# Optimization experiments

Hardware: AMD Instinct MI355X
Metric: run time of the kernel (lower is better)

The kernel has to match this reference:

```python
import jax, jax.numpy as jnp
import numpy as np

EPS = 1e-5  # BatchNorm eps
K_NN = 16


def _conv1d(w, b, x):
    # 1x1 Conv1d: w (O,C), x (B,C,N) -> (B,O,N)
    return jnp.einsum('oc,bcn->bon', w, x) + b[None, :, None]


def _conv2d(w, b, x):
    # 1x1 Conv2d: w (O,C), x (B,C,N,K) -> (B,O,N,K)
    return jnp.einsum('oc,bcnk->bonk', w, x) + b[None, :, None, None]


def _bn2d(x, g, bt, mu, var):
    # eval-mode BatchNorm2d over channel axis 1
    inv = g / jnp.sqrt(var + EPS)
    return x * inv[None, :, None, None] + (bt - mu * inv)[None, :, None, None]


def _group(f, idx):
    # grouping_operation: f (B,C,M), idx (B,N,K) -> (B,C,N,K)
    return jax.vmap(lambda fb, ib: fb[:, ib])(f, idx)


def _knn(query_pts, ref_pts, k):
    # query (B,N,3), ref (B,M,3) -> k nearest ref indices per query (B,N,k)
    d = (jnp.sum(query_pts ** 2, -1)[:, :, None]
         + jnp.sum(ref_pts ** 2, -1)[:, None, :]
         - 2.0 * jnp.einsum('bnc,bmc->bnm', query_pts, ref_pts))
    _, idx = jax.lax.top_k(-d, k)
    return idx


def setup_inputs() -> dict:
    key = jax.random.key(0)
    B, n, m, C, D, PH = 4, 4096, 1024, 128, 256, 64
    AH = 2 * D
    ks = iter(jax.random.split(key, 40))

    def nrm(shape, scale):
        return jax.random.normal(next(ks), shape, jnp.float32) * scale

    pos = nrm((B, 3, n), 1.0)
    return {
        'pos': pos,
        'pos_flipped': jnp.transpose(pos, (0, 2, 1)),
        'fea': nrm((B, C, n), 1.0),
        'seed': nrm((B, m, 3), 1.0),
        'seed_fea': nrm((B, C, m), 1.0),
        'w_start': nrm((D, C), C ** -0.5), 'b_start': jnp.zeros((D,), jnp.float32),
        'w_key': nrm((D, D), D ** -0.5), 'b_key': jnp.zeros((D,), jnp.float32),
        'w_value': nrm((D, D), D ** -0.5), 'b_value': jnp.zeros((D,), jnp.float32),
        'w_query': nrm((D, C), C ** -0.5), 'b_query': jnp.zeros((D,), jnp.float32),
        'pos_w1': nrm((PH, 4), 0.5), 'pos_b1': jnp.zeros((PH,), jnp.float32),
        'pos_g1': jnp.ones((PH,), jnp.float32), 'pos_beta1': jnp.zeros((PH,), jnp.float32),
        'pos_mu1': jnp.zeros((PH,), jnp.float32), 'pos_var1': jnp.ones((PH,), jnp.float32),
        'pos_w2': nrm((D, PH), PH ** -0.5), 'pos_b2': jnp.zeros((D,), jnp.float32),
        'attn_w1': nrm((AH, D), D ** -0.5), 'attn_b1': jnp.zeros((AH,), jnp.float32),
        'attn_g1': jnp.ones((AH,), jnp.float32), 'attn_beta1': jnp.zeros((AH,), jnp.float32),
        'attn_mu1': jnp.zeros((AH,), jnp.float32), 'attn_var1': jnp.ones((AH,), jnp.float32),
        'attn_w2': nrm((D, AH), AH ** -0.5), 'attn_b2': jnp.zeros((D,), jnp.float32),
        'w_end': nrm((C, D), D ** -0.5), 'b_end': jnp.zeros((C,), jnp.float32),
    }


def reference(pos, pos_flipped, fea, seed, seed_fea,
              w_start, b_start, w_key, b_key, w_value, b_value, w_query, b_query,
              pos_w1, pos_b1, pos_g1, pos_beta1, pos_mu1, pos_var1, pos_w2, pos_b2,
              attn_w1, attn_b1, attn_g1, attn_beta1, attn_mu1, attn_var1, attn_w2, attn_b2,
              w_end, b_end):
    value = _conv1d(w_start, b_start, seed_fea)                    # (B,D,m)
    idx = _knn(jax.lax.stop_gradient(pos_flipped),
               jax.lax.stop_gradient(seed), K_NN)                  # (B,n,K) no-grad topk
    key_f = _conv1d(w_key, b_key, value)
    val_f = _conv1d(w_value, b_value, value)
    query = _conv1d(w_query, b_query, fea)                         # (B,D,n)
    key_g = _group(key_f, idx)                                     # (B,D,n,K)
    qk_rel = query[:, :, :, None] - key_g
    val_g = _group(val_f, idx)                                     # (B,D,n,K)
    coord_xj = _group(jnp.transpose(seed, (0, 2, 1)), idx)         # (B,3,n,K)
    pos_rel = pos[:, :, :, None] - coord_xj                        # (B,3,n,K)
    dis = jnp.linalg.norm(pos_rel, axis=1, keepdims=True)          # (B,1,n,K)
    h = jnp.concatenate([dis, pos_rel], axis=1)                    # (B,4,n,K)
    pe = _conv2d(pos_w2, pos_b2,
                 jax.nn.relu(_bn2d(_conv2d(pos_w1, pos_b1, h),
                                   pos_g1, pos_beta1, pos_mu1, pos_var1)))  # (B,D,n,K)
    hid = jax.nn.relu(_bn2d(_conv2d(attn_w1, attn_b1, qk_rel + pe),
                            attn_g1, attn_beta1, attn_mu1, attn_var1))
    weights = jax.nn.softmax(_conv2d(attn_w2, attn_b2, hid), axis=-1)  # softmax over K
    agg = jnp.einsum('bcnk,bcnk->bcn', weights, val_g + pe)        # (B,D,n)
    return _conv1d(w_end, b_end, agg) + fea                        # (B,C,n)
```

## Files before the change

kernel.cpp:

```cpp
#include <hip/hip_runtime.h>
#include <hip/hip_bf16.h>

#define BB   4
#define NQ   4096
#define MS   1024
#define CF   128
#define DD   256
#define PHH  64
#define AHH  512
#define KNN  16
#define EPSBN 1e-5f
#define LDH  72
#define LKH  264

typedef unsigned short ushort_t;
typedef __attribute__((ext_vector_type(8))) short bf16x8;
typedef __attribute__((ext_vector_type(4))) float floatx4;

__device__ __forceinline__ float u2f(ushort_t u) {
  return __uint_as_float(((unsigned int)u) << 16);
}
__device__ __forceinline__ ushort_t f2u(float f) {
  __hip_bfloat16 h = __float2bfloat16(f);
  return *(ushort_t*)&h;
}

#define NSEG 30
struct CvtArgs {
  const void* src[NSEG];
  int cnt[NSEG];
  int off[NSEG];
};

__global__ __launch_bounds__(256) void cvt_kernel(CvtArgs a, float* __restrict__ dst,
                                                  const ushort_t* __restrict__ probe) {
  const bool f32 = (probe[0] == 0);
  const int gid = blockIdx.x * 256 + threadIdx.x;
  const int gsz = gridDim.x * 256;
  for (int s = 0; s < NSEG; ++s) {
    float* d = dst + a.off[s];
    const int n = a.cnt[s];
    if (f32) {
      const float* sp = (const float*)a.src[s];
      for (int i = gid; i < n; i += gsz) d[i] = sp[i];
    } else {
      const ushort_t* sp = (const ushort_t*)a.src[s];
      for (int i = gid; i < n; i += gsz) d[i] = u2f(sp[i]);
    }
  }
}

__global__ __launch_bounds__(256) void cvtw_kernel(
    const float* __restrict__ w1f, const float* __restrict__ w2f,
    const float* __restrict__ w2pf,
    ushort_t* __restrict__ w1b, ushort_t* __restrict__ w2b,
    ushort_t* __restrict__ w2pb) {
  int i = blockIdx.x * 256 + threadIdx.x;
  w1b[i] = f2u(w1f[i]);
  w2b[i] = f2u(w2f[i]);
  if (i < DD * PHH) w2pb[i] = f2u(w2pf[i]);
}

__global__ __launch_bounds__(128) void prep_kernel(
    const float* __restrict__ w1f, const float* __restrict__ w2pf,
    const float* __restrict__ wqf, const float* __restrict__ bqf,
    const float* __restrict__ b2f, const float* __restrict__ ab1f,
    ushort_t* __restrict__ WWb, ushort_t* __restrict__ WQHb,
    float* __restrict__ ballf) {
  __shared__ float s_w1[DD];
  const int a = blockIdx.x;
  const int t = threadIdx.x;
  s_w1[t] = w1f[a * DD + t];
  s_w1[t + 128] = w1f[a * DD + t + 128];
  __syncthreads();
  {
    float acc = 0.f;
    for (int d = 0; d < DD; ++d) acc += s_w1[d] * wqf[d * CF + t];
    WQHb[a * CF + t] = f2u(acc);
  }
  if (t < PHH) {
    float acc = 0.f;
    for (int d = 0; d < DD; ++d) acc += s_w1[d] * w2pf[d * PHH + t];
    WWb[a * PHH + t] = f2u(acc);
  }
  if (t == 0) {
    float acc = ab1f[a];
    for (int d = 0; d < DD; ++d) acc += s_w1[d] * (bqf[d] + b2f[d]);
    ballf[a] = acc;
  }
}

__global__ __launch_bounds__(256) void vkv_kernel(
    const float* __restrict__ w_start, const float* __restrict__ b_start,
    const float* __restrict__ w_key, const float* __restrict__ b_key,
    const float* __restrict__ w_value, const float* __restrict__ b_value,
    const float* __restrict__ seed_fea,
    ushort_t* __restrict__ key_b, ushort_t* __restrict__ val_b) {
  __shared__ __align__(16) float s_val[4][DD];
  const int tid = threadIdx.x;
  const int b = blockIdx.x >> 8;
  const int m0 = (blockIdx.x & 255) << 2;

  float a0 = b_start[tid], a1 = a0, a2 = a0, a3 = a0;
  {
    const float* wrow = w_start + tid * CF;
    const float* colb = seed_fea + b * CF * MS + m0;
    for (int c = 0; c < CF; c += 4) {
      float4 w = *(const float4*)(wrow + c);
      float4 f0 = *(const float4*)(colb + (c + 0) * MS);
      float4 f1 = *(const float4*)(colb + (c + 1) * MS);
      float4 f2 = *(const float4*)(colb + (c + 2) * MS);
      float4 f3 = *(const float4*)(colb + (c + 3) * MS);
      a0 += w.x * f0.x + w.y * f1.x + w.z * f2.x + w.w * f3.x;
      a1 += w.x * f0.y + w.y * f1.y + w.z * f2.y + w.w * f3.y;
      a2 += w.x * f0.z + w.y * f1.z + w.z * f2.z + w.w * f3.z;
      a3 += w.x * f0.w + w.y * f1.w + w.z * f2.w + w.w * f3.w;
    }
  }
  s_val[0][tid] = a0; s_val[1][tid] = a1; s_val[2][tid] = a2; s_val[3][tid] = a3;
  __syncthreads();

  float ak[4], av[4];
#pragma unroll
  for (int i = 0; i < 4; ++i) { ak[i] = b_key[tid]; av[i] = b_value[tid]; }
  {
    const float* kr = w_key + tid * DD;
    const float* vr = w_value + tid * DD;
    for (int c = 0; c < DD; c += 4) {
      float4 ku = *(const float4*)(kr + c);
      float4 vu = *(const float4*)(vr + c);
      float4 v0 = *(const float4*)(&s_val[0][c]);
      float4 v1 = *(const float4*)(&s_val[1][c]);
      float4 v2 = *(const float4*)(&s_val[2][c]);
      float4 v3 = *(const float4*)(&s_val[3][c]);
      ak[0] += ku.x * v0.x + ku.y * v0.y + ku.z * v0.z + ku.w * v0.w;
      ak[1] += ku.x * v1.x + ku.y * v1.y + ku.z * v1.z + ku.w * v1.w;
      ak[2] += ku.x * v2.x + ku.y * v2.y + ku.z * v2.z + ku.w * v2.w;
      ak[3] += ku.x * v3.x + ku.y * v3.y + ku.z * v3.z + ku.w * v3.w;
      av[0] += vu.x * v0.x + vu.y * v0.y + vu.z * v0.z + vu.w * v0.w;
      av[1] += vu.x * v1.x + vu.y * v1.y + vu.z * v1.z + vu.w * v1.w;
      av[2] += vu.x * v2.x + vu.y * v2.y + vu.z * v2.z + vu.w * v2.w;
      av[3] += vu.x * v3.x + vu.y * v3.y + vu.z * v3.z + vu.w * v3.w;
    }
  }
#pragma unroll
  for (int i = 0; i < 4; ++i) {
    key_b[(b * MS + m0 + i) * DD + tid] = f2u(ak[i]);
    val_b[(b * MS + m0 + i) * DD + tid] = f2u(av[i]);
  }
}

__global__ __launch_bounds__(256) void kh_kernel(
    const ushort_t* __restrict__ key_b, const ushort_t* __restrict__ w1b,
    ushort_t* __restrict__ khb) {
  __shared__ __align__(16) ushort_t s_key[16 * LKH];
  const int tid = threadIdx.x;
  const int wv = tid >> 6, ln = tid & 63;
  const int qu = ln >> 4, l15 = ln & 15;
  const int b = blockIdx.x >> 6;
  const int m0 = (blockIdx.x & 63) << 4;
  {
    const int row = tid >> 4, seg = tid & 15;
    const ushort_t* src = key_b + (b * MS + m0 + row) * DD + seg * 16;
    ushort_t* dst = s_key + row * LKH + seg * 16;
    *(bf16x8*)(dst + 0) = *(const bf16x8*)(src + 0);
    *(bf16x8*)(dst + 8) = *(const bf16x8*)(src + 8);
  }
  __syncthreads();
  bf16x8 af[8];
#pragma unroll
  for (int ks = 0; ks < 8; ++ks)
    af[ks] = *(const bf16x8*)(s_key + l15 * LKH + ks * 32 + qu * 8);
  floatx4 acc[8];
#pragma unroll
  for (int nt = 0; nt < 8; ++nt) acc[nt] = (floatx4){0.f, 0.f, 0.f, 0.f};
#pragma unroll
  for (int ks = 0; ks < 8; ++ks)
#pragma unroll
    for (int nt = 0; nt < 8; ++nt) {
      bf16x8 bfr = *(const bf16x8*)(w1b + (wv * 128 + nt * 16 + l15) * DD + ks * 32 + qu * 8);
      acc[nt] = __builtin_amdgcn_mfma_f32_16x16x32_bf16(af[ks], bfr, acc[nt], 0, 0, 0);
    }
#pragma unroll
  for (int nt = 0; nt < 8; ++nt)
#pragma unroll
    for (int r = 0; r < 4; ++r)
      khb[(b * MS + m0 + qu * 4 + r) * AHH + wv * 128 + nt * 16 + l15] = f2u(acc[nt][r]);
}

__global__ __launch_bounds__(512) void knn_kernel(
    const float* __restrict__ pos_flipped, const float* __restrict__ seed,
    int* __restrict__ idx_out) {
  __shared__ float s_p[MS * 3];
  const int tid = threadIdx.x;
  const int wv = tid >> 6, ln = tid & 63;
  const int b = blockIdx.x >> 9;
  const int q = ((blockIdx.x & 511) << 3) + wv;

  for (int i = tid; i < MS * 3; i += 512) s_p[i] = seed[b * MS * 3 + i];
  __syncthreads();

  const float qx = pos_flipped[(b * NQ + q) * 3 + 0];
  const float qy = pos_flipped[(b * NQ + q) * 3 + 1];
  const float qz = pos_flipped[(b * NQ + q) * 3 + 2];
  const float q2 = qx * qx + qy * qy + qz * qz;

  unsigned long long key[16];
#pragma unroll
  for (int t = 0; t < 16; ++t) {
    int j = ln + (t << 6);
    float x = s_p[j * 3 + 0], y = s_p[j * 3 + 1], z = s_p[j * 3 + 2];
    float r2 = x * x + y * y + z * z;
    float dist = q2 + r2 - 2.0f * (qx * x + qy * y + qz * z);
    unsigned u = __float_as_uint(dist);
    u ^= (u >> 31) ? 0xFFFFFFFFu : 0x80000000u;
    key[t] = ((unsigned long long)u << 10) | (unsigned)j;
  }

#pragma unroll 1
  for (int r = 0; r < KNN; ++r) {
    unsigned long long m = key[0];
#pragma unroll
    for (int t = 1; t < 16; ++t) m = (key[t] < m) ? key[t] : m;
#pragma unroll
    for (int off = 32; off >= 1; off >>= 1) {
      unsigned lo = (unsigned)m, hi = (unsigned)(m >> 32);
      unsigned olo = __shfl_xor((int)lo, off);
      unsigned ohi = __shfl_xor((int)hi, off);
      unsigned long long o = ((unsigned long long)ohi << 32) | olo;
      m = (o < m) ? o : m;
    }
    if (ln == 0) idx_out[(b * NQ + q) * KNN + r] = (int)(m & 1023u);
#pragma unroll
    for (int t = 0; t < 16; ++t) key[t] = (key[t] == m) ? ~0ull : key[t];
  }
}

__global__ __launch_bounds__(256, 4) void fused_kernel(
    const float* __restrict__ pos, const float* __restrict__ seed,
    const void* __restrict__ fea_raw,
    const float* __restrict__ pos_w1, const float* __restrict__ pos_b1,
    const float* __restrict__ pos_g1, const float* __restrict__ pos_beta1,
    const float* __restrict__ pos_mu1, const float* __restrict__ pos_var1,
    const ushort_t* __restrict__ w2pb, const float* __restrict__ pos_b2,
    const float* __restrict__ attn_g1, const float* __restrict__ attn_beta1,
    const float* __restrict__ attn_mu1, const float* __restrict__ attn_var1,
    const float* __restrict__ ballf,
    const ushort_t* __restrict__ WWb, const ushort_t* __restrict__ WQHb,
    const ushort_t* __restrict__ w2b, const ushort_t* __restrict__ khb,
    const ushort_t* __restrict__ val_b,
    const int* __restrict__ idx_in,
    const float* __restrict__ w_end, const float* __restrict__ b_end,
    void* __restrict__ out_raw, const ushort_t* __restrict__ probe) {
  __shared__ __align__(16) ushort_t s_phb[64 * LDH];
  __shared__ __align__(16) ushort_t s_hid[64 * LDH];
  __shared__ __align__(16) float s_qh[4 * AHH];
  __shared__ __align__(16) ushort_t s_feab[4 * CF];
  __shared__ float s_h[64 * 4];
  __shared__ int s_idx[64];

  float* s_agg = s_qh;

  const int tid = threadIdx.x;
  const int wv = tid >> 6;
  const int ln = tid & 63;
  const int qu = ln >> 4, l15 = ln & 15;
  const bool f32io = (probe[0] == 0);
  const int q0 = blockIdx.x * 4;
  const int b = q0 >> 12;
  const int qn0 = q0 & (NQ - 1);

  if (tid < 64) {
    const int g = tid >> 4;
    const int qn = qn0 + g;
    const int j = idx_in[(q0 + g) * KNN + (tid & 15)];
    s_idx[tid] = j;
    float px = pos[(b * 3 + 0) * NQ + qn];
    float py = pos[(b * 3 + 1) * NQ + qn];
    float pz = pos[(b * 3 + 2) * NQ + qn];
    float rx = px - seed[(b * MS + j) * 3 + 0];
    float ry = py - seed[(b * MS + j) * 3 + 1];
    float rz = pz - seed[(b * MS + j) * 3 + 2];
    float dis = sqrtf(rx * rx + ry * ry + rz * rz);
    s_h[tid * 4 + 0] = dis;
    s_h[tid * 4 + 1] = rx;
    s_h[tid * 4 + 2] = ry;
    s_h[tid * 4 + 3] = rz;
  }
  if (tid < 128) {
    const int c = tid;
    if (f32io) {
      const float* fc = (const float*)fea_raw + (size_t)b * CF * NQ + (size_t)c * NQ + qn0;
      float4 v = *(const float4*)fc;
      s_feab[0 * CF + c] = f2u(v.x);
      s_feab[1 * CF + c] = f2u(v.y);
      s_feab[2 * CF + c] = f2u(v.z);
      s_feab[3 * CF + c] = f2u(v.w);
    } else {
      const ushort_t* fc = (const ushort_t*)fea_raw + (size_t)b * CF * NQ + (size_t)c * NQ + qn0;
      unsigned long long v = *(const unsigned long long*)fc;
      s_feab[0 * CF + c] = (ushort_t)(v);
      s_feab[1 * CF + c] = (ushort_t)(v >> 16);
      s_feab[2 * CF + c] = (ushort_t)(v >> 32);
      s_feab[3 * CF + c] = (ushort_t)(v >> 48);
    }
  }
  __syncthreads();

  {
    const int p = tid & 63, kb = tid >> 6;
    float4 w = *(const float4*)(pos_w1 + p * 4);
    float inv = pos_g1[p] * rsqrtf(pos_var1[p] + EPSBN);
    float off = pos_b1[p] * inv + pos_beta1[p] - pos_mu1[p] * inv;
#pragma unroll
    for (int i = 0; i < 16; ++i) {
      int gk = kb * 16 + i;
      float raw = w.x * s_h[gk * 4 + 0] + w.y * s_h[gk * 4 + 1] +
                  w.z * s_h[gk * 4 + 2] + w.w * s_h[gk * 4 + 3];
      s_phb[gk * LDH + p] = f2u(fmaxf(raw * inv + off, 0.0f));
    }
  }

  {
    bf16x8 afq[4];
#pragma unroll
    for (int ks = 0; ks < 4; ++ks) {
      if (l15 < 4) afq[ks] = *(const bf16x8*)(s_feab + l15 * CF + ks * 32 + qu * 8);
      else afq[ks] = (bf16x8){0, 0, 0, 0, 0, 0, 0, 0};
    }
    floatx4 aq[8];
#pragma unroll
    for (int nt = 0; nt < 8; ++nt) aq[nt] = (floatx4){0.f, 0.f, 0.f, 0.f};
#pragma unroll
    for (int ks = 0; ks < 4; ++ks)
#pragma unroll
      for (int nt = 0; nt < 8; ++nt) {
        bf16x8 bfr = *(const bf16x8*)(WQHb + (nt * 64 + wv * 16 + l15) * CF + ks * 32 + qu * 8);
        aq[nt] = __builtin_amdgcn_mfma_f32_16x16x32_bf16(afq[ks], bfr, aq[nt], 0, 0, 0);
      }
    if (qu == 0) {
#pragma unroll
      for (int nt = 0; nt < 8; ++nt)
#pragma unroll
        for (int r = 0; r < 4; ++r)
          s_qh[r * AHH + nt * 64 + wv * 16 + l15] = aq[nt][r];
    }
  }
  __syncthreads();

  floatx4 accl[4][4];
#pragma unroll
  for (int mt = 0; mt < 4; ++mt)
#pragma unroll
    for (int nt = 0; nt < 4; ++nt) accl[mt][nt] = (floatx4){0.f, 0.f, 0.f, 0.f};

#pragma unroll 1
  for (int nc = 0; nc < 8; ++nc) {
    {
      floatx4 accb[4];
#pragma unroll
      for (int mt = 0; mt < 4; ++mt) accb[mt] = (floatx4){0.f, 0.f, 0.f, 0.f};
#pragma unroll
      for (int ks = 0; ks < 2; ++ks) {
        bf16x8 bw = *(const bf16x8*)(WWb + (nc * 64 + wv * 16 + l15) * PHH + ks * 32 + qu * 8);
#pragma unroll
        for (int mt = 0; mt < 4; ++mt) {
          bf16x8 af = *(const bf16x8*)(s_phb + (mt * 16 + l15) * LDH + ks * 32 + qu * 8);
          accb[mt] = __builtin_amdgcn_mfma_f32_16x16x32_bf16(af, bw, accb[mt], 0, 0, 0);
        }
      }
      const int a = nc * 64 + wv * 16 + l15;
      float inv = attn_g1[a] * rsqrtf(attn_var1[a] + EPSBN);
      float offc = ballf[a] * inv + attn_beta1[a] - attn_mu1[a] * inv;
#pragma unroll
      for (int mt = 0; mt < 4; ++mt) {
        const float qhv = s_qh[mt * AHH + a];
#pragma unroll
        for (int r = 0; r < 4; ++r) {
          const int row = mt * 16 + qu * 4 + r;
          float khv = u2f(khb[(b * MS + s_idx[row]) * AHH + a]);
          float raw = accb[mt][r] + qhv - khv;
          s_hid[row * LDH + wv * 16 + l15] = f2u(fmaxf(raw * inv + offc, 0.0f));
        }
      }
    }
    __syncthreads();
    {
#pragma unroll
      for (int ks = 0; ks < 2; ++ks) {
        bf16x8 af2[4];
#pragma unroll
        for (int mt = 0; mt < 4; ++mt)
          af2[mt] = *(const bf16x8*)(s_hid + (mt * 16 + l15) * LDH + ks * 32 + qu * 8);
#pragma unroll
        for (int nt = 0; nt < 4; ++nt) {
          bf16x8 bfr = *(const bf16x8*)(w2b + (wv * 64 + nt * 16 + l15) * AHH +
                                        nc * 64 + ks * 32 + qu * 8);
#pragma unroll
          for (int mt = 0; mt < 4; ++mt)
            accl[mt][nt] = __builtin_amdgcn_mfma_f32_16x16x32_bf16(af2[mt], bfr, accl[mt][nt], 0, 0, 0);
        }
      }
    }
    __syncthreads();
  }

#pragma unroll
  for (int nt = 0; nt < 4; ++nt) {
    const int c = wv * 64 + nt * 16 + l15;
    floatx4 ap[4];
#pragma unroll
    for (int mt = 0; mt < 4; ++mt) ap[mt] = (floatx4){0.f, 0.f, 0.f, 0.f};
#pragma unroll
    for (int ks = 0; ks < 2; ++ks) {
      bf16x8 bfr = *(const bf16x8*)(w2pb + c * PHH + ks * 32 + qu * 8);
#pragma unroll
      for (int mt = 0; mt < 4; ++mt) {
        bf16x8 af = *(const bf16x8*)(s_phb + (mt * 16 + l15) * LDH + ks * 32 + qu * 8);
        ap[mt] = __builtin_amdgcn_mfma_f32_16x16x32_bf16(af, bfr, ap[mt], 0, 0, 0);
      }
    }
    const float b2v = pos_b2[c];
#pragma unroll
    for (int mt = 0; mt < 4; ++mt) {
      float l0 = accl[mt][nt][0], l1 = accl[mt][nt][1];
      float l2 = accl[mt][nt][2], l3 = accl[mt][nt][3];
      float mx = fmaxf(fmaxf(l0, l1), fmaxf(l2, l3));
      mx = fmaxf(mx, __shfl_xor(mx, 16));
      mx = fmaxf(mx, __shfl_xor(mx, 32));
      float e0 = expf(l0 - mx), e1 = expf(l1 - mx);
      float e2 = expf(l2 - mx), e3 = expf(l3 - mx);
      float s = e0 + e1 + e2 + e3;
      s += __shfl_xor(s, 16);
      s += __shfl_xor(s, 32);
      const int row0 = mt * 16 + qu * 4;
      float v0 = u2f(val_b[(b * MS + s_idx[row0 + 0]) * DD + c]);
      float v1 = u2f(val_b[(b * MS + s_idx[row0 + 1]) * DD + c]);
      float v2 = u2f(val_b[(b * MS + s_idx[row0 + 2]) * DD + c]);
      float v3 = u2f(val_b[(b * MS + s_idx[row0 + 3]) * DD + c]);
      float p = e0 * (v0 + ap[mt][0] + b2v) + e1 * (v1 + ap[mt][1] + b2v) +
                e2 * (v2 + ap[mt][2] + b2v) + e3 * (v3 + ap[mt][3] + b2v);
      p += __shfl_xor(p, 16);
      p += __shfl_xor(p, 32);
      if (ln < 16) s_agg[mt * DD + c] = p / s;
    }
  }
  __syncthreads();

  {
    const int c = tid & 127;
    const int qh = tid >> 7;
    float acc0 = 0.0f, acc1 = 0.0f;
    const float* wr = w_end + c * DD;
    for (int d = 0; d < DD; d += 4) {
      float4 w4 = *(const float4*)(wr + d);
      float4 a0 = *(const float4*)(s_agg + (qh + 0) * DD + d);
      float4 a1 = *(const float4*)(s_agg + (qh + 2) * DD + d);
      acc0 += w4.x * a0.x + w4.y * a0.y + w4.z * a0.z + w4.w * a0.w;
      acc1 += w4.x * a1.x + w4.y * a1.y + w4.z * a1.z + w4.w * a1.w;
    }
    const float be = b_end[c];
#pragma unroll
    for (int t = 0; t < 2; ++t) {
      const int q = qh + t * 2;
      const float accv = (t == 0) ? acc0 : acc1;
      const int oidx = (b * CF + c) * NQ + qn0 + q;
      float fres = f32io ? ((const float*)fea_raw)[oidx]
                         : u2f(((const ushort_t*)fea_raw)[oidx]);
      float v = accv + be + fres;
      if (f32io) ((float*)out_raw)[oidx] = v;
      else ((ushort_t*)out_raw)[oidx] = f2u(v);
    }
  }
}

extern "C" void kernel_launch(void* const* d_in, const int* in_sizes, int n_in,
                              void* d_out, int out_size, void* d_ws, size_t ws_size,
                              hipStream_t stream) {
  (void)in_sizes; (void)n_in; (void)out_size; (void)ws_size;

  float* wsf = (float*)d_ws;
  ushort_t* key_b = (ushort_t*)wsf;
  ushort_t* val_b = (ushort_t*)(wsf + 524288);
  int*      idxw  = (int*)(wsf + 1048576);
  float*    nrm   = wsf + 1310720;
  ushort_t* w1b   = (ushort_t*)(wsf + 2458304);
  ushort_t* w2b   = (ushort_t*)(wsf + 2523840);
  ushort_t* w2pb  = (ushort_t*)(wsf + 2589376);
  ushort_t* khb   = (ushort_t*)(wsf + 2613952);
  ushort_t* WWb   = (ushort_t*)(wsf + 3662528);
  ushort_t* WQHb  = (ushort_t*)(wsf + 3678912);
  float*    ballf = wsf + 3711680;

  static const int seg_in[NSEG] = {0, 1, 3, 4, 5, 6, 7, 8, 9, 10, 11, 12, 13, 14,
                                   15, 16, 17, 18, 19, 20, 21, 22, 23, 24, 25, 26,
                                   27, 28, 29, 30};
  static const int seg_cnt[NSEG] = {
      49152, 49152, 12288, 524288, 32768, 256, 65536, 256, 65536, 256,
      32768, 256, 256, 64, 64, 64, 64, 64, 16384, 256,
      131072, 512, 512, 512, 512, 512, 131072, 256, 32768, 128};
  static const int seg_off[NSEG] = {
      0, 49152, 98304, 110592, 634880, 667648, 667904, 733440, 733696, 799232,
      799488, 832256, 832512, 832768, 832832, 832896, 832960, 833024, 833088, 849472,
      849728, 980800, 981312, 981824, 982336, 982848, 983360, 1114432, 1114688, 1147456};

  CvtArgs ca;
  for (int s = 0; s < NSEG; ++s) {
    ca.src[s] = d_in[seg_in[s]];
    ca.cnt[s] = seg_cnt[s];
    ca.off[s] = seg_off[s];
  }
  const ushort_t* probe = (const ushort_t*)d_in[18];

  const float* posN      = nrm + 0;
  const float* pos_flipN = nrm + 49152;
  const float* seedN     = nrm + 98304;
  const float* seed_feaN = nrm + 110592;
  const float* w_startN  = nrm + 634880;
  const float* b_startN  = nrm + 667648;
  const float* w_keyN    = nrm + 667904;
  const float* b_keyN    = nrm + 733440;
  const float* w_valueN  = nrm + 733696;
  const float* b_valueN  = nrm + 799232;
  const float* w_queryN  = nrm + 799488;
  const float* b_queryN  = nrm + 832256;
  const float* pos_w1N   = nrm + 832512;
  const float* pos_b1N   = nrm + 832768;
  const float* pos_g1N   = nrm + 832832;
  const float* pos_beta1N= nrm + 832896;
  const float* pos_mu1N  = nrm + 832960;
  const float* pos_var1N = nrm + 833024;
  const float* pos_w2N   = nrm + 833088;
  const float* pos_b2N   = nrm + 849472;
  const float* attn_w1N  = nrm + 849728;
  const float* attn_b1N  = nrm + 980800;
  const float* attn_g1N  = nrm + 981312;
  const float* attn_beta1N = nrm + 981824;
  const float* attn_mu1N = nrm + 982336;
  const float* attn_var1N= nrm + 982848;
  const float* attn_w2N  = nrm + 983360;
  const float* w_endN    = nrm + 1114688;
  const float* b_endN    = nrm + 1147456;

  cvt_kernel<<<512, 256, 0, stream>>>(ca, nrm, probe);
  cvtw_kernel<<<512, 256, 0, stream>>>(attn_w1N, attn_w2N, pos_w2N,
                                       w1b, w2b, w2pb);
  prep_kernel<<<512, 128, 0, stream>>>(attn_w1N, pos_w2N, w_queryN,
                                       b_queryN, pos_b2N, attn_b1N,
                                       WWb, WQHb, ballf);
  vkv_kernel<<<BB * MS / 4, 256, 0, stream>>>(w_startN, b_startN, w_keyN, b_keyN,
                                              w_valueN, b_valueN, seed_feaN,
                                              key_b, val_b);
  kh_kernel<<<BB * MS / 16, 256, 0, stream>>>(key_b, w1b, khb);
  knn_kernel<<<BB * NQ / 8, 512, 0, stream>>>(pos_flipN, seedN, idxw);

  fused_kernel<<<BB * NQ / 4, 256, 0, stream>>>(
      posN, seedN, d_in[2],
      pos_w1N, pos_b1N, pos_g1N, pos_beta1N, pos_mu1N, pos_var1N,
      w2pb, pos_b2N,
      attn_g1N, attn_beta1N, attn_mu1N, attn_var1N,
      ballf, WWb, WQHb, w2b, khb, val_b, idxw,
      w_endN, b_endN, d_out, probe);
}
```

Baseline: 747.6 us.

## Prefetch gathered key-hidden values one chunk ahead and raise occupancy bound

The gathered khb loads for the next hidden-channel chunk are now issued before the second GEMM of the current chunk. The values are packed two bf16 per register, and the loop is manually unrolled by two with ping-pong buffers. This is meant to hide the latency of the scattered global gather behind MFMA work. Launch bounds also move from 4 to 5 blocks per CU. That caps registers tighter and risks spills, especially with the extra prefetch registers and the 64-entry accl accumulators.

```diff
diff --git a/kernel.cpp b/kernel.cpp
--- a/kernel.cpp
+++ b/kernel.cpp
@@ -236,7 +236,7 @@
   }
 }
 
-__global__ __launch_bounds__(256, 4) void fused_kernel(
+__global__ __launch_bounds__(256, 5) void fused_kernel(
     const float* __restrict__ pos, const float* __restrict__ seed,
     const void* __restrict__ fea_raw,
     const float* __restrict__ pos_w1, const float* __restrict__ pos_b1,
@@ -354,54 +354,84 @@
 #pragma unroll
     for (int nt = 0; nt < 4; ++nt) accl[mt][nt] = (floatx4){0.f, 0.f, 0.f, 0.f};
 
+  auto ldkh = [&](int nc, unsigned (&pk)[8]) {
+    const int a = nc * 64 + wv * 16 + l15;
+#pragma unroll
+    for (int mt = 0; mt < 4; ++mt)
+#pragma unroll
+      for (int rp = 0; rp < 2; ++rp) {
+        const int row = mt * 16 + qu * 4 + rp * 2;
+        unsigned lo = khb[(b * MS + s_idx[row]) * AHH + a];
+        unsigned hi = khb[(b * MS + s_idx[row + 1]) * AHH + a];
+        pk[mt * 2 + rp] = lo | (hi << 16);
+      }
+  };
+
+  auto do_B = [&](int nc, const unsigned (&pk)[8]) {
+    floatx4 accb[4];
+#pragma unroll
+    for (int mt = 0; mt < 4; ++mt) accb[mt] = (floatx4){0.f, 0.f, 0.f, 0.f};
+#pragma unroll
+    for (int ks = 0; ks < 2; ++ks) {
+      bf16x8 bw = *(const bf16x8*)(WWb + (nc * 64 + wv * 16 + l15) * PHH + ks * 32 + qu * 8);
+#pragma unroll
+      for (int mt = 0; mt < 4; ++mt) {
+        bf16x8 af = *(const bf16x8*)(s_phb + (mt * 16 + l15) * LDH + ks * 32 + qu * 8);
+        accb[mt] = __builtin_amdgcn_mfma_f32_16x16x32_bf16(af, bw, accb[mt], 0, 0, 0);
+      }
+    }
+    const int a = nc * 64 + wv * 16 + l15;
+    float inv = attn_g1[a] * rsqrtf(attn_var1[a] + EPSBN);
+    float offc = ballf[a] * inv + attn_beta1[a] - attn_mu1[a] * inv;
+#pragma unroll
+    for (int mt = 0; mt < 4; ++mt) {
+      const float qhv = s_qh[mt * AHH + a];
+#pragma unroll
+      for (int rp = 0; rp < 2; ++rp) {
+        const float kh0 = u2f((ushort_t)(pk[mt * 2 + rp] & 0xFFFFu));
+        const float kh1 = u2f((ushort_t)(pk[mt * 2 + rp] >> 16));
+        const int row0 = mt * 16 + qu * 4 + rp * 2;
+        float raw0 = accb[mt][rp * 2 + 0] + qhv - kh0;
+        float raw1 = accb[mt][rp * 2 + 1] + qhv - kh1;
+        s_hid[(row0 + 0) * LDH + wv * 16 + l15] = f2u(fmaxf(raw0 * inv + offc, 0.0f));
+        s_hid[(row0 + 1) * LDH + wv * 16 + l15] = f2u(fmaxf(raw1 * inv + offc, 0.0f));
+      }
+    }
+  };
+
+  auto do_C = [&](int nc) {
+#pragma unroll
+    for (int ks = 0; ks < 2; ++ks) {
+      bf16x8 af2[4];
+#pragma unroll
+      for (int mt = 0; mt < 4; ++mt)
+        af2[mt] = *(const bf16x8*)(s_hid + (mt * 16 + l15) * LDH + ks * 32 + qu * 8);
+#pragma unroll
+      for (int nt = 0; nt < 4; ++nt) {
+        bf16x8 bfr = *(const bf16x8*)(w2b + (wv * 64 + nt * 16 + l15) * AHH +
+                                      nc * 64 + ks * 32 + qu * 8);
+#pragma unroll
+        for (int mt = 0; mt < 4; ++mt)
+          accl[mt][nt] = __builtin_amdgcn_mfma_f32_16x16x32_bf16(af2[mt], bfr, accl[mt][nt], 0, 0, 0);
+      }
+    }
+  };
+
+  unsigned pkA[8], pkB[8];
+  ldkh(0, pkA);
+
 #pragma unroll 1
-  for (int nc = 0; nc < 8; ++nc) {
-    {
-      floatx4 accb[4];
-#pragma unroll
-      for (int mt = 0; mt < 4; ++mt) accb[mt] = (floatx4){0.f, 0.f, 0.f, 0.f};
-#pragma unroll
-      for (int ks = 0; ks < 2; ++ks) {
-        bf16x8 bw = *(const bf16x8*)(WWb + (nc * 64 + wv * 16 + l15) * PHH + ks * 32 + qu * 8);
-#pragma unroll
-        for (int mt = 0; mt < 4; ++mt) {
-          bf16x8 af = *(const bf16x8*)(s_phb + (mt * 16 + l15) * LDH + ks * 32 + qu * 8);
-          accb[mt] = __builtin_amdgcn_mfma_f32_16x16x32_bf16(af, bw, accb[mt], 0, 0, 0);
-        }
-      }
-      const int a = nc * 64 + wv * 16 + l15;
-      float inv = attn_g1[a] * rsqrtf(attn_var1[a] + EPSBN);
-      float offc = ballf[a] * inv + attn_beta1[a] - attn_mu1[a] * inv;
-#pragma unroll
-      for (int mt = 0; mt < 4; ++mt) {
-        const float qhv = s_qh[mt * AHH + a];
-#pragma unroll
-        for (int r = 0; r < 4; ++r) {
-          const int row = mt * 16 + qu * 4 + r;
-          float khv = u2f(khb[(b * MS + s_idx[row]) * AHH + a]);
-          float raw = accb[mt][r] + qhv - khv;
-          s_hid[row * LDH + wv * 16 + l15] = f2u(fmaxf(raw * inv + offc, 0.0f));
-        }
-      }
-    }
+  for (int pr = 0; pr < 4; ++pr) {
+    const int nc0 = pr * 2, nc1 = pr * 2 + 1;
+    do_B(nc0, pkA);
     __syncthreads();
-    {
-#pragma unroll
-      for (int ks = 0; ks < 2; ++ks) {
-        bf16x8 af2[4];
-#pragma unroll
-        for (int mt = 0; mt < 4; ++mt)
-          af2[mt] = *(const bf16x8*)(s_hid + (mt * 16 + l15) * LDH + ks * 32 + qu * 8);
-#pragma unroll
-        for (int nt = 0; nt < 4; ++nt) {
-          bf16x8 bfr = *(const bf16x8*)(w2b + (wv * 64 + nt * 16 + l15) * AHH +
-                                        nc * 64 + ks * 32 + qu * 8);
-#pragma unroll
-          for (int mt = 0; mt < 4; ++mt)
-            accl[mt][nt] = __builtin_amdgcn_mfma_f32_16x16x32_bf16(af2[mt], bfr, accl[mt][nt], 0, 0, 0);
-        }
-      }
-    }
+    ldkh(nc1, pkB);
+    do_C(nc0);
+    __syncthreads();
+    do_B(nc1, pkB);
+    __syncthreads();
+    if (pr < 3) ldkh(nc0 + 2, pkA);
+    do_C(nc1);
     __syncthreads();
   }
 
```

New measurement: 1.317 ms. +76.1%, slower.

## Double-buffer attention hidden tile to overlap stage B and C across chunks

Applied to the files above, without the earlier changes.

Splits the shared hidden buffer into two and software-pipelines the 8-chunk loop, so chunk nc+1's first-layer MFMA and BN/ReLU is computed into one buffer while chunk nc's second-layer MFMA reads the other. This halves the block barriers per chunk and lets the gather loads of khb overlap with MFMA work. It costs an extra 9 KB of LDS per block, which may reduce occupancy under the 4-blocks-per-CU launch bound, and raises register pressure from holding both stages live.

```diff
diff --git a/kernel.cpp b/kernel.cpp
--- a/kernel.cpp
+++ b/kernel.cpp
@@ -236,6 +236,63 @@
   }
 }
 
+#define DO_B(NCX, HID)                                                         \
+  {                                                                            \
+    const int nc_ = (NCX);                                                     \
+    floatx4 accb[4];                                                           \
+    _Pragma("unroll")                                                          \
+    for (int mt = 0; mt < 4; ++mt) accb[mt] = (floatx4){0.f, 0.f, 0.f, 0.f};   \
+    _Pragma("unroll")                                                          \
+    for (int ks = 0; ks < 2; ++ks) {                                           \
+      bf16x8 bw = *(const bf16x8*)(WWb + (nc_ * 64 + wv * 16 + l15) * PHH +    \
+                                   ks * 32 + qu * 8);                          \
+      _Pragma("unroll")                                                        \
+      for (int mt = 0; mt < 4; ++mt) {                                         \
+        bf16x8 af = *(const bf16x8*)(s_phb + (mt * 16 + l15) * LDH +           \
+                                     ks * 32 + qu * 8);                        \
+        accb[mt] = __builtin_amdgcn_mfma_f32_16x16x32_bf16(af, bw, accb[mt],   \
+                                                           0, 0, 0);           \
+      }                                                                        \
+    }                                                                          \
+    const int a_ = nc_ * 64 + wv * 16 + l15;                                   \
+    float inv_ = attn_g1[a_] * rsqrtf(attn_var1[a_] + EPSBN);                  \
+    float offc_ = ballf[a_] * inv_ + attn_beta1[a_] - attn_mu1[a_] * inv_;     \
+    _Pragma("unroll")                                                          \
+    for (int mt = 0; mt < 4; ++mt) {                                           \
+      const float qhv_ = s_qh[mt * AHH + a_];                                  \
+      _Pragma("unroll")                                                        \
+      for (int r = 0; r < 4; ++r) {                                            \
+        const int row_ = mt * 16 + qu * 4 + r;                                 \
+        float khv_ = u2f(khb[(b * MS + s_idx[row_]) * AHH + a_]);              \
+        float raw_ = accb[mt][r] + qhv_ - khv_;                                \
+        (HID)[row_ * LDH + wv * 16 + l15] =                                    \
+            f2u(fmaxf(raw_ * inv_ + offc_, 0.0f));                             \
+      }                                                                        \
+    }                                                                          \
+  }
+
+#define DO_C(NCX, HID)                                                         \
+  {                                                                            \
+    const int nc_ = (NCX);                                                     \
+    _Pragma("unroll")                                                          \
+    for (int ks = 0; ks < 2; ++ks) {                                           \
+      bf16x8 af2[4];                                                           \
+      _Pragma("unroll")                                                        \
+      for (int mt = 0; mt < 4; ++mt)                                           \
+        af2[mt] = *(const bf16x8*)((HID) + (mt * 16 + l15) * LDH +             \
+                                   ks * 32 + qu * 8);                          \
+      _Pragma("unroll")                                                        \
+      for (int nt = 0; nt < 4; ++nt) {                                         \
+        bf16x8 bfr = *(const bf16x8*)(w2b + (wv * 64 + nt * 16 + l15) * AHH +  \
+                                      nc_ * 64 + ks * 32 + qu * 8);            \
+        _Pragma("unroll")                                                      \
+        for (int mt = 0; mt < 4; ++mt)                                         \
+          accl[mt][nt] = __builtin_amdgcn_mfma_f32_16x16x32_bf16(              \
+              af2[mt], bfr, accl[mt][nt], 0, 0, 0);                            \
+      }                                                                        \
+    }                                                                          \
+  }
+
 __global__ __launch_bounds__(256, 4) void fused_kernel(
     const float* __restrict__ pos, const float* __restrict__ seed,
     const void* __restrict__ fea_raw,
@@ -253,7 +310,8 @@
     const float* __restrict__ w_end, const float* __restrict__ b_end,
     void* __restrict__ out_raw, const ushort_t* __restrict__ probe) {
   __shared__ __align__(16) ushort_t s_phb[64 * LDH];
-  __shared__ __align__(16) ushort_t s_hid[64 * LDH];
+  __shared__ __align__(16) ushort_t s_hid0[64 * LDH];
+  __shared__ __align__(16) ushort_t s_hid1[64 * LDH];
   __shared__ __align__(16) float s_qh[4 * AHH];
   __shared__ __align__(16) ushort_t s_feab[4 * CF];
   __shared__ float s_h[64 * 4];
@@ -354,54 +412,15 @@
 #pragma unroll
     for (int nt = 0; nt < 4; ++nt) accl[mt][nt] = (floatx4){0.f, 0.f, 0.f, 0.f};
 
+  DO_B(0, s_hid0);
+  __syncthreads();
+
 #pragma unroll 1
   for (int nc = 0; nc < 8; ++nc) {
-    {
-      floatx4 accb[4];
-#pragma unroll
-      for (int mt = 0; mt < 4; ++mt) accb[mt] = (floatx4){0.f, 0.f, 0.f, 0.f};
-#pragma unroll
-      for (int ks = 0; ks < 2; ++ks) {
-        bf16x8 bw = *(const bf16x8*)(WWb + (nc * 64 + wv * 16 + l15) * PHH + ks * 32 + qu * 8);
-#pragma unroll
-        for (int mt = 0; mt < 4; ++mt) {
-          bf16x8 af = *(const bf16x8*)(s_phb + (mt * 16 + l15) * LDH + ks * 32 + qu * 8);
-          accb[mt] = __builtin_amdgcn_mfma_f32_16x16x32_bf16(af, bw, accb[mt], 0, 0, 0);
-        }
-      }
-      const int a = nc * 64 + wv * 16 + l15;
-      float inv = attn_g1[a] * rsqrtf(attn_var1[a] + EPSBN);
-      float offc = ballf[a] * inv + attn_beta1[a] - attn_mu1[a] * inv;
-#pragma unroll
-      for (int mt = 0; mt < 4; ++mt) {
-        const float qhv = s_qh[mt * AHH + a];
-#pragma unroll
-        for (int r = 0; r < 4; ++r) {
-          const int row = mt * 16 + qu * 4 + r;
-          float khv = u2f(khb[(b * MS + s_idx[row]) * AHH + a]);
-          float raw = accb[mt][r] + qhv - khv;
-          s_hid[row * LDH + wv * 16 + l15] = f2u(fmaxf(raw * inv + offc, 0.0f));
-        }
-      }
-    }
-    __syncthreads();
-    {
-#pragma unroll
-      for (int ks = 0; ks < 2; ++ks) {
-        bf16x8 af2[4];
-#pragma unroll
-        for (int mt = 0; mt < 4; ++mt)
-          af2[mt] = *(const bf16x8*)(s_hid + (mt * 16 + l15) * LDH + ks * 32 + qu * 8);
-#pragma unroll
-        for (int nt = 0; nt < 4; ++nt) {
-          bf16x8 bfr = *(const bf16x8*)(w2b + (wv * 64 + nt * 16 + l15) * AHH +
-                                        nc * 64 + ks * 32 + qu * 8);
-#pragma unroll
-          for (int mt = 0; mt < 4; ++mt)
-            accl[mt][nt] = __builtin_amdgcn_mfma_f32_16x16x32_bf16(af2[mt], bfr, accl[mt][nt], 0, 0, 0);
-        }
-      }
-    }
+    ushort_t* cur = (nc & 1) ? s_hid1 : s_hid0;
+    ushort_t* nxt = (nc & 1) ? s_hid0 : s_hid1;
+    if (nc < 7) DO_B(nc + 1, nxt);
+    DO_C(nc, cur);
     __syncthreads();
   }
 
```

After: 730.6 us (median of 2 runs). 2.3% less time.
